# Kernel optimization log

Measured on AMD Instinct MI355X. Metric: run time of the kernel, lower is better.

The kernel has to match this reference:

```python
import jax, jax.numpy as jnp
import numpy as np

C = 256
H = 8
D = C // H


def setup_inputs() -> dict:
    key = jax.random.key(0)
    ks = jax.random.split(key, 6)
    scale = 1.0 / np.sqrt(C)
    x = jax.random.normal(ks[0], (8, C, 2048), dtype=jnp.float32)
    Wq = jax.random.normal(ks[1], (C, C), dtype=jnp.float32) * scale
    Wk = jax.random.normal(ks[2], (C, C), dtype=jnp.float32) * scale
    Wv = jax.random.normal(ks[3], (C, C), dtype=jnp.float32) * scale
    Wo = jax.random.normal(ks[4], (C, C), dtype=jnp.float32) * scale
    bo = jax.random.normal(ks[5], (C,), dtype=jnp.float32) * 0.01
    return {"x": x, "Wq": Wq, "Wk": Wk, "Wv": Wv, "Wo": Wo, "bo": bo}


def reference(x, Wq, Wk, Wv, Wo, bo):
    # x: [N, C, L]; Conv1d(k=1) == per-position matmul with weight [out, in]
    q = jnp.einsum('oc,ncl->nol', Wq, x)
    k = jnp.einsum('oc,ncl->nol', Wk, x)
    v = jnp.einsum('oc,ncl->nol', Wv, x)
    N, _, L = x.shape
    # rearrange 'n (h d) l -> n l h d'
    q = q.reshape(N, H, D, L).transpose(0, 3, 1, 2)
    k = k.reshape(N, H, D, L).transpose(0, 3, 1, 2)
    v = v.reshape(N, H, D, L).transpose(0, 3, 1, 2)
    qk = jnp.einsum('nqhd,nkhd->nhqk', q, k)
    # NOTE: original scales by full embedding size (channels), not head_dim
    attn = jax.nn.softmax(qk * (C ** -0.5), axis=3)
    out = jnp.einsum('nhql,nlhd->nqhd', attn, v)
    # rearrange 'n l h d -> n (h d) l'
    out = out.transpose(0, 2, 3, 1).reshape(N, C, L)
    return jnp.einsum('oc,ncl->nol', Wo, out) + bo[None, :, None]
```

## Files before the change

kernel.cpp:

```cpp
#include <hip/hip_runtime.h>


typedef __bf16 bf8 __attribute__((ext_vector_type(8)));
typedef float f4 __attribute__((ext_vector_type(4)));
typedef float f32x4 __attribute__((ext_vector_type(4)));
typedef unsigned short u16;
typedef unsigned int u32;
typedef u16 u16x4 __attribute__((ext_vector_type(4)));
typedef u16 u16x8 __attribute__((ext_vector_type(8)));
typedef u32 u32x2 __attribute__((ext_vector_type(2)));

__device__ __forceinline__ u16 f2bf(float f) {
  __bf16 h = (__bf16)f;
  return __builtin_bit_cast(u16, h);
}
__device__ __forceinline__ float bf2f(u16 b) {
  union { u32 u; float f; } v; v.u = ((u32)b) << 16;
  return v.f;
}
__device__ __forceinline__ u32 pk2bf(float a, float b) {
  return ((u32)f2bf(b) << 16) | (u32)f2bf(a);
}
__device__ __forceinline__ u32 pktrunc(float a, float b) {
  return __builtin_amdgcn_perm(__builtin_bit_cast(u32, b),
                               __builtin_bit_cast(u32, a), 0x07060302u);
}
__device__ __forceinline__ float exp2_fast(float x) {
  return __builtin_amdgcn_exp2f(x);
}

#define MFMA(a, b, c) __builtin_amdgcn_mfma_f32_16x16x32_bf16((a), (b), (c), 0, 0, 0)

union bf8u { u32 u[4]; bf8 v; };
__device__ __forceinline__ bf8 mkbf8(u32 a, u32 b, u32 c, u32 d) {
  bf8u t; t.u[0] = a; t.u[1] = b; t.u[2] = c; t.u[3] = d; return t.v;
}

__global__ __launch_bounds__(256) void convert_weights(
    const float* __restrict__ Wq, const float* __restrict__ Wk,
    const float* __restrict__ Wv, const float* __restrict__ Wo,
    const float* __restrict__ bo,
    u16* __restrict__ Wqb, u16* __restrict__ Wkb, u16* __restrict__ Wvb,
    u16* __restrict__ Wob, u16* __restrict__ bob) {
  const int tid = threadIdx.x;
  const int seg = blockIdx.x >> 6;
  const int blk = blockIdx.x & 63;
  const float* s; u16* d;
  if (seg == 0)      { s = Wq; d = Wqb; }
  else if (seg == 1) { s = Wk; d = Wkb; }
  else if (seg == 2) { s = Wv; d = Wvb; }
  else               { s = Wo; d = Wob; }
  const int base = blk * 1024 + tid * 4;
  f32x4 v = *(const f32x4*)(s + base);
  u16x4 o;
#pragma unroll
  for (int i = 0; i < 4; ++i) o[i] = f2bf(v[i]);
  *(u16x4*)(d + base) = o;
  if (blockIdx.x == 0 && tid < 64) {
    const int bb = tid * 4;
    f32x4 bv = *(const f32x4*)(bo + bb);
    u16x4 ob;
#pragma unroll
    for (int i = 0; i < 4; ++i) ob[i] = f2bf(bv[i]);
    *(u16x4*)(bob + bb) = ob;
  }
}

__global__ __launch_bounds__(256) void qkv_proj(
    const float* __restrict__ x, const u16* __restrict__ Wq,
    const u16* __restrict__ Wk, const u16* __restrict__ Wv,
    u16* __restrict__ qbuf, u16* __restrict__ kbuf, u16* __restrict__ vbuf) {
  __shared__ __align__(16) u16 xt[2][64 * 40];
  const int n = blockIdx.z;
  const int o0 = blockIdx.y * 64;
  const int l0 = blockIdx.x * 64;
  const int tid = threadIdx.x;
  const int w = tid >> 6, lane = tid & 63, quad = lane >> 4, l16 = lane & 15;
  const int ow = o0 + w * 16;
  const float SC = 0.09019327066650391f;

  f4 acc[3][4];
#pragma unroll
  for (int p = 0; p < 3; ++p)
#pragma unroll
    for (int lt = 0; lt < 4; ++lt) acc[p][lt] = (f4){0.f, 0.f, 0.f, 0.f};

  const int cp = tid >> 4;
  const int lq = (tid & 15) * 4;

  auto stage = [&](int c0, int buf) {
    const float* xp = x + (n * 256 + c0 + 2 * cp) * 2048 + l0 + lq;
    f32x4 r0 = *(const f32x4*)xp;
    f32x4 r1 = *(const f32x4*)(xp + 2048);
#pragma unroll
    for (int i = 0; i < 4; ++i)
      *(u32*)&xt[buf][(lq + i) * 40 + 2 * cp] = pk2bf(r0[i], r1[i]);
  };

  stage(0, 0);
  for (int s = 0; s < 8; ++s) {
    __syncthreads();
    if (s < 7) stage((s + 1) * 32, (s + 1) & 1);
    const int c0 = s * 32;
    bf8 a0 = *(const bf8*)(Wq + (ow + l16) * 256 + c0 + quad * 8);
    bf8 a1 = *(const bf8*)(Wk + (ow + l16) * 256 + c0 + quad * 8);
    bf8 a2 = *(const bf8*)(Wv + (ow + l16) * 256 + c0 + quad * 8);
    const u16* xb = xt[s & 1];
#pragma unroll
    for (int lt = 0; lt < 4; ++lt) {
      bf8 b = *(const bf8*)&xb[(lt * 16 + l16) * 40 + quad * 8];
      acc[0][lt] = MFMA(a0, b, acc[0][lt]);
      acc[1][lt] = MFMA(a1, b, acc[1][lt]);
      acc[2][lt] = MFMA(a2, b, acc[2][lt]);
    }
  }
  const int hh = ow >> 5;
  const int dbase = (ow & 31) + quad * 4;
#pragma unroll
  for (int lt = 0; lt < 4; ++lt) {
    const int l = l0 + lt * 16 + l16;
    const size_t base = ((size_t)(n * 8 + hh) * 2048 + l) * 32 + dbase;
    u16x4 qv, kv;
#pragma unroll
    for (int r = 0; r < 4; ++r) {
      qv[r] = f2bf(acc[0][lt][r] * SC);
      kv[r] = f2bf(acc[1][lt][r]);
    }
    *(u16x4*)(qbuf + base) = qv;
    *(u16x4*)(kbuf + base) = kv;
#pragma unroll
    for (int r = 0; r < 4; ++r)
      vbuf[(n * 256 + ow + quad * 4 + r) * 2048 + l] = f2bf(acc[2][lt][r]);
  }
}

__global__ __launch_bounds__(64) void attn(
    const u16* __restrict__ qbuf, const u16* __restrict__ kbuf,
    const u16* __restrict__ vbuf, u16* __restrict__ abuf) {
  const int head = blockIdx.x, qblk = blockIdx.y;
  const int n = head >> 3, h = head & 7;
  const int lane = threadIdx.x;
  const int quad = lane >> 4, l16 = lane & 15;
  const int q0 = qblk * 64;

  const u16* kb = kbuf + (size_t)head * 2048 * 32 + l16 * 32 + quad * 8;
  const u16* vb = vbuf + ((size_t)n * 256 + h * 32) * 2048;

  const bf8 ones = mkbf8(0x3F803F80u, 0x3F803F80u, 0x3F803F80u, 0x3F803F80u);

  bf8 aq[4];
#pragma unroll
  for (int qt = 0; qt < 4; ++qt)
    aq[qt] = *(const bf8*)(qbuf + ((size_t)head * 2048 + q0 + qt * 16 + l16) * 32 + quad * 8);

  f4 O[2][4];
  f4 Lacc[4];
#pragma unroll
  for (int qt = 0; qt < 4; ++qt) {
    O[0][qt] = (f4){0.f, 0.f, 0.f, 0.f};
    O[1][qt] = (f4){0.f, 0.f, 0.f, 0.f};
    Lacc[qt] = (f4){0.f, 0.f, 0.f, 0.f};
  }

  bf8 bk[4];
  u32x2 vf[8];
#pragma unroll
  for (int kt = 0; kt < 4; ++kt) bk[kt] = *(const bf8*)(kb + kt * 16 * 32);
#pragma unroll
  for (int dt = 0; dt < 2; ++dt)
#pragma unroll
    for (int kt = 0; kt < 4; ++kt)
      vf[dt * 4 + kt] = *(const u32x2*)(vb + (dt * 16 + l16) * 2048 + kt * 16 + quad * 4);

  for (int kc = 0; kc < 2048; kc += 64) {
    const int kn = (kc < 1984) ? kc + 64 : 0;
    bf8 nk[4];
    u32x2 nv[8];
#pragma unroll
    for (int kt = 0; kt < 4; ++kt) nk[kt] = *(const bf8*)(kb + (kn + kt * 16) * 32);
#pragma unroll
    for (int dt = 0; dt < 2; ++dt)
#pragma unroll
      for (int kt = 0; kt < 4; ++kt)
        nv[dt * 4 + kt] = *(const u32x2*)(vb + (dt * 16 + l16) * 2048 + kn + kt * 16 + quad * 4);

#pragma unroll
    for (int qt = 0; qt < 4; ++qt) {
      f4 z = (f4){0.f, 0.f, 0.f, 0.f};
      f4 s0 = MFMA(bk[0], aq[qt], z);
      f4 s1 = MFMA(bk[1], aq[qt], z);
      f4 s2 = MFMA(bk[2], aq[qt], z);
      f4 s3 = MFMA(bk[3], aq[qt], z);
      f4 e0, e1, e2, e3;
#pragma unroll
      for (int r = 0; r < 4; ++r) {
        e0[r] = exp2_fast(s0[r]);
        e1[r] = exp2_fast(s1[r]);
        e2[r] = exp2_fast(s2[r]);
        e3[r] = exp2_fast(s3[r]);
      }
      bf8 B0 = mkbf8(pktrunc(e0[0], e0[1]), pktrunc(e0[2], e0[3]),
                     pktrunc(e1[0], e1[1]), pktrunc(e1[2], e1[3]));
      bf8 B1 = mkbf8(pktrunc(e2[0], e2[1]), pktrunc(e2[2], e2[3]),
                     pktrunc(e3[0], e3[1]), pktrunc(e3[2], e3[3]));
      Lacc[qt] = MFMA(ones, B0, Lacc[qt]);
      Lacc[qt] = MFMA(ones, B1, Lacc[qt]);
#pragma unroll
      for (int dt = 0; dt < 2; ++dt) {
        bf8 A0 = mkbf8(vf[dt * 4 + 0][0], vf[dt * 4 + 0][1],
                       vf[dt * 4 + 1][0], vf[dt * 4 + 1][1]);
        bf8 A1 = mkbf8(vf[dt * 4 + 2][0], vf[dt * 4 + 2][1],
                       vf[dt * 4 + 3][0], vf[dt * 4 + 3][1]);
        f4 o = O[dt][qt];
        o = MFMA(A0, B0, o);
        o = MFMA(A1, B1, o);
        O[dt][qt] = o;
      }
    }
#pragma unroll
    for (int i = 0; i < 4; ++i) bk[i] = nk[i];
#pragma unroll
    for (int i = 0; i < 8; ++i) vf[i] = nv[i];
  }

#pragma unroll
  for (int qt = 0; qt < 4; ++qt) {
    const float inv = 1.0f / Lacc[qt][0];
    const int q = q0 + qt * 16 + l16;
#pragma unroll
    for (int dt = 0; dt < 2; ++dt) {
      u16x4 ov;
#pragma unroll
      for (int r = 0; r < 4; ++r) ov[r] = f2bf(O[dt][qt][r] * inv);
      *(u16x4*)(abuf + ((size_t)n * 2048 + q) * 256 + h * 32 + dt * 16 + quad * 4) = ov;
    }
  }
}

__global__ __launch_bounds__(256) void out_proj(
    const u16* __restrict__ abuf, const u16* __restrict__ Wo,
    const u16* __restrict__ bo, float* __restrict__ out) {
  const int n = blockIdx.z;
  const int o0 = blockIdx.y * 64;
  const int l0 = blockIdx.x * 64;
  const int tid = threadIdx.x;
  const int w = tid >> 6, lane = tid & 63, quad = lane >> 4, l16 = lane & 15;
  const int ow = o0 + w * 16;

  const u16* wp = Wo + (ow + l16) * 256 + quad * 8;
  const u16* ab = abuf + ((size_t)n * 2048 + l0 + l16) * 256 + quad * 8;

  f4 acc[4];
#pragma unroll
  for (int lt = 0; lt < 4; ++lt) acc[lt] = (f4){0.f, 0.f, 0.f, 0.f};

  bf8 a = *(const bf8*)wp;
  bf8 b[4];
#pragma unroll
  for (int lt = 0; lt < 4; ++lt) b[lt] = *(const bf8*)(ab + lt * 16 * 256);

  for (int c0 = 0; c0 < 256; c0 += 32) {
    const int cn = (c0 < 224) ? c0 + 32 : 0;
    bf8 na = *(const bf8*)(wp + cn);
    bf8 nb[4];
#pragma unroll
    for (int lt = 0; lt < 4; ++lt)
      nb[lt] = *(const bf8*)(ab + lt * 16 * 256 + cn);
#pragma unroll
    for (int lt = 0; lt < 4; ++lt) acc[lt] = MFMA(a, b[lt], acc[lt]);
    a = na;
#pragma unroll
    for (int lt = 0; lt < 4; ++lt) b[lt] = nb[lt];
  }
#pragma unroll
  for (int r = 0; r < 4; ++r) {
    const int o = ow + quad * 4 + r;
    const float bias = bf2f(bo[o]);
#pragma unroll
    for (int lt = 0; lt < 4; ++lt) {
      out[((size_t)n * 256 + o) * 2048 + l0 + lt * 16 + l16] = acc[lt][r] + bias;
    }
  }
}

extern "C" void kernel_launch(void* const* d_in, const int* in_sizes, int n_in,
                              void* d_out, int out_size, void* d_ws, size_t ws_size,
                              hipStream_t stream) {
  const float* x  = (const float*)d_in[0];
  const float* Wq = (const float*)d_in[1];
  const float* Wk = (const float*)d_in[2];
  const float* Wv = (const float*)d_in[3];
  const float* Wo = (const float*)d_in[4];
  const float* bo = (const float*)d_in[5];
  float* out = (float*)d_out;

  u16* ws = (u16*)d_ws;
  u16* qbuf = ws;
  u16* kbuf = qbuf + 4194304;
  u16* vbuf = kbuf + 4194304;
  u16* abuf = vbuf + 4194304;
  u16* Wqb  = abuf + 4194304;
  u16* Wkb  = Wqb + 65536;
  u16* Wvb  = Wkb + 65536;
  u16* Wob  = Wvb + 65536;
  u16* bob  = Wob + 65536;

  convert_weights<<<dim3(256), 256, 0, stream>>>(Wq, Wk, Wv, Wo, bo,
                                                 Wqb, Wkb, Wvb, Wob, bob);
  qkv_proj<<<dim3(32, 4, 8), 256, 0, stream>>>(x, Wqb, Wkb, Wvb,
                                               qbuf, kbuf, vbuf);
  attn<<<dim3(64, 32), 64, 0, stream>>>(qbuf, kbuf, vbuf, abuf);
  out_proj<<<dim3(32, 4, 8), 256, 0, stream>>>(abuf, Wob, bob, out);
}
```

Measured before the change: 191.3 us.

## Split attention key range across four waves and permute V layout for bf8 loads

```diff
diff --git a/kernel.cpp b/kernel.cpp
--- a/kernel.cpp
+++ b/kernel.cpp
@@ -8,7 +8,6 @@
 typedef unsigned int u32;
 typedef u16 u16x4 __attribute__((ext_vector_type(4)));
 typedef u16 u16x8 __attribute__((ext_vector_type(8)));
-typedef u32 u32x2 __attribute__((ext_vector_type(2)));
 
 __device__ __forceinline__ u16 f2bf(float f) {
   __bf16 h = (__bf16)f;
@@ -119,6 +118,7 @@
 #pragma unroll
   for (int lt = 0; lt < 4; ++lt) {
     const int l = l0 + lt * 16 + l16;
+    const int vpos = l0 + (lt >> 1) * 32 + (l16 >> 2) * 8 + (l16 & 3) + (lt & 1) * 4;
     const size_t base = ((size_t)(n * 8 + hh) * 2048 + l) * 32 + dbase;
     u16x4 qv, kv;
 #pragma unroll
@@ -130,21 +130,24 @@
     *(u16x4*)(kbuf + base) = kv;
 #pragma unroll
     for (int r = 0; r < 4; ++r)
-      vbuf[(n * 256 + ow + quad * 4 + r) * 2048 + l] = f2bf(acc[2][lt][r]);
-  }
-}
-
-__global__ __launch_bounds__(64) void attn(
+      vbuf[(n * 256 + ow + quad * 4 + r) * 2048 + vpos] = f2bf(acc[2][lt][r]);
+  }
+}
+
+__global__ __launch_bounds__(256) void attn(
     const u16* __restrict__ qbuf, const u16* __restrict__ kbuf,
     const u16* __restrict__ vbuf, u16* __restrict__ abuf) {
+  __shared__ float Osh[3][64][37];
   const int head = blockIdx.x, qblk = blockIdx.y;
   const int n = head >> 3, h = head & 7;
-  const int lane = threadIdx.x;
+  const int tid = threadIdx.x;
+  const int w = tid >> 6, lane = tid & 63;
   const int quad = lane >> 4, l16 = lane & 15;
   const int q0 = qblk * 64;
+  const int kc0 = w * 512;
 
   const u16* kb = kbuf + (size_t)head * 2048 * 32 + l16 * 32 + quad * 8;
-  const u16* vb = vbuf + ((size_t)n * 256 + h * 32) * 2048;
+  const u16* vb = vbuf + ((size_t)n * 256 + h * 32 + l16) * 2048 + quad * 8;
 
   const bf8 ones = mkbf8(0x3F803F80u, 0x3F803F80u, 0x3F803F80u, 0x3F803F80u);
 
@@ -162,27 +165,25 @@
     Lacc[qt] = (f4){0.f, 0.f, 0.f, 0.f};
   }
 
-  bf8 bk[4];
-  u32x2 vf[8];
-#pragma unroll
-  for (int kt = 0; kt < 4; ++kt) bk[kt] = *(const bf8*)(kb + kt * 16 * 32);
+  bf8 bk[4], vf[4];
+#pragma unroll
+  for (int kt = 0; kt < 4; ++kt) bk[kt] = *(const bf8*)(kb + (kc0 + kt * 16) * 32);
 #pragma unroll
   for (int dt = 0; dt < 2; ++dt)
 #pragma unroll
-    for (int kt = 0; kt < 4; ++kt)
-      vf[dt * 4 + kt] = *(const u32x2*)(vb + (dt * 16 + l16) * 2048 + kt * 16 + quad * 4);
-
-  for (int kc = 0; kc < 2048; kc += 64) {
-    const int kn = (kc < 1984) ? kc + 64 : 0;
-    bf8 nk[4];
-    u32x2 nv[8];
+    for (int g = 0; g < 2; ++g)
+      vf[dt * 2 + g] = *(const bf8*)(vb + dt * 16 * 2048 + kc0 + g * 32);
+
+  for (int kc = kc0; kc < kc0 + 512; kc += 64) {
+    const int kn = (kc < kc0 + 448) ? kc + 64 : kc0;
+    bf8 nk[4], nv[4];
 #pragma unroll
     for (int kt = 0; kt < 4; ++kt) nk[kt] = *(const bf8*)(kb + (kn + kt * 16) * 32);
 #pragma unroll
     for (int dt = 0; dt < 2; ++dt)
 #pragma unroll
-      for (int kt = 0; kt < 4; ++kt)
-        nv[dt * 4 + kt] = *(const u32x2*)(vb + (dt * 16 + l16) * 2048 + kn + kt * 16 + quad * 4);
+      for (int g = 0; g < 2; ++g)
+        nv[dt * 2 + g] = *(const bf8*)(vb + dt * 16 * 2048 + kn + g * 32);
 
 #pragma unroll
     for (int qt = 0; qt < 4; ++qt) {
@@ -207,32 +208,54 @@
       Lacc[qt] = MFMA(ones, B1, Lacc[qt]);
 #pragma unroll
       for (int dt = 0; dt < 2; ++dt) {
-        bf8 A0 = mkbf8(vf[dt * 4 + 0][0], vf[dt * 4 + 0][1],
-                       vf[dt * 4 + 1][0], vf[dt * 4 + 1][1]);
-        bf8 A1 = mkbf8(vf[dt * 4 + 2][0], vf[dt * 4 + 2][1],
-                       vf[dt * 4 + 3][0], vf[dt * 4 + 3][1]);
         f4 o = O[dt][qt];
-        o = MFMA(A0, B0, o);
-        o = MFMA(A1, B1, o);
+        o = MFMA(vf[dt * 2 + 0], B0, o);
+        o = MFMA(vf[dt * 2 + 1], B1, o);
         O[dt][qt] = o;
       }
     }
 #pragma unroll
-    for (int i = 0; i < 4; ++i) bk[i] = nk[i];
-#pragma unroll
-    for (int i = 0; i < 8; ++i) vf[i] = nv[i];
-  }
-
-#pragma unroll
-  for (int qt = 0; qt < 4; ++qt) {
-    const float inv = 1.0f / Lacc[qt][0];
-    const int q = q0 + qt * 16 + l16;
-#pragma unroll
-    for (int dt = 0; dt < 2; ++dt) {
-      u16x4 ov;
-#pragma unroll
-      for (int r = 0; r < 4; ++r) ov[r] = f2bf(O[dt][qt][r] * inv);
-      *(u16x4*)(abuf + ((size_t)n * 2048 + q) * 256 + h * 32 + dt * 16 + quad * 4) = ov;
+    for (int i = 0; i < 4; ++i) { bk[i] = nk[i]; vf[i] = nv[i]; }
+  }
+
+  if (w > 0) {
+#pragma unroll
+    for (int dt = 0; dt < 2; ++dt)
+#pragma unroll
+      for (int qt = 0; qt < 4; ++qt)
+#pragma unroll
+        for (int r = 0; r < 4; ++r)
+          Osh[w - 1][lane][dt * 16 + qt * 4 + r] = O[dt][qt][r];
+#pragma unroll
+    for (int qt = 0; qt < 4; ++qt)
+      Osh[w - 1][lane][32 + qt] = Lacc[qt][0];
+  }
+  __syncthreads();
+  if (w == 0) {
+#pragma unroll
+    for (int p = 0; p < 3; ++p) {
+#pragma unroll
+      for (int dt = 0; dt < 2; ++dt)
+#pragma unroll
+        for (int qt = 0; qt < 4; ++qt)
+#pragma unroll
+          for (int r = 0; r < 4; ++r)
+            O[dt][qt][r] += Osh[p][lane][dt * 16 + qt * 4 + r];
+#pragma unroll
+      for (int qt = 0; qt < 4; ++qt)
+        Lacc[qt][0] += Osh[p][lane][32 + qt];
+    }
+#pragma unroll
+    for (int qt = 0; qt < 4; ++qt) {
+      const float inv = 1.0f / Lacc[qt][0];
+      const int q = q0 + qt * 16 + l16;
+#pragma unroll
+      for (int dt = 0; dt < 2; ++dt) {
+        u16x4 ov;
+#pragma unroll
+        for (int r = 0; r < 4; ++r) ov[r] = f2bf(O[dt][qt][r] * inv);
+        *(u16x4*)(abuf + ((size_t)n * 2048 + q) * 256 + h * 32 + dt * 16 + quad * 4) = ov;
+      }
     }
   }
 }
@@ -309,6 +332,6 @@
                                                  Wqb, Wkb, Wvb, Wob, bob);
   qkv_proj<<<dim3(32, 4, 8), 256, 0, stream>>>(x, Wqb, Wkb, Wvb,
                                                qbuf, kbuf, vbuf);
-  attn<<<dim3(64, 32), 64, 0, stream>>>(qbuf, kbuf, vbuf, abuf);
+  attn<<<dim3(64, 32), 256, 0, stream>>>(qbuf, kbuf, vbuf, abuf);
   out_proj<<<dim3(32, 4, 8), 256, 0, stream>>>(abuf, Wob, bob, out);
 }
```

Result: faster. 173.3 us (-9.4%).
